# Optimization experiments

Measured on AMD Instinct MI355X. Metric: run time of the kernel, lower is better.

## Reference

```python
import jax, jax.numpy as jnp
import numpy as np

N_NODES = 50000
N_EDGES = 800000
IN_DIM = 128
HID = 128
N_GRAPHS = 256
N_CLASSES = 2
ALPHA = 0.2  # leaky relu slope
EPS_BN = 1e-5


def setup_inputs() -> dict:
    key = jax.random.key(0)
    ks = jax.random.split(key, 24)
    adjacency = jax.random.randint(ks[0], (2, N_EDGES), 0, N_NODES, dtype=jnp.int32)
    input_feature = jax.random.normal(ks[1], (N_NODES, IN_DIM), dtype=jnp.float32)
    graph_indicator = jnp.sort(jax.random.randint(ks[2], (N_NODES,), 0, N_GRAPHS, dtype=jnp.int32))
    labels = jax.random.randint(ks[3], (N_GRAPHS,), 0, N_CLASSES, dtype=jnp.int64)
    s = 0.05
    params = {
        'W1': jax.random.normal(ks[4], (IN_DIM, HID), jnp.float32) * s,
        'a1': jax.random.normal(ks[5], (2 * HID,), jnp.float32) * s,
        'bn2_g': jnp.ones((HID,), jnp.float32),
        'bn2_b': jnp.zeros((HID,), jnp.float32),
        'W2': jax.random.normal(ks[6], (HID, HID), jnp.float32) * s,
        'a2': jax.random.normal(ks[7], (2 * HID,), jnp.float32) * s,
        'bn3_g': jnp.ones((HID,), jnp.float32),
        'bn3_b': jnp.zeros((HID,), jnp.float32),
        'W3': jax.random.normal(ks[8], (HID, HID), jnp.float32) * s,
        'a3': jax.random.normal(ks[9], (2 * HID,), jnp.float32) * s,
        'fc1_w': jax.random.normal(ks[10], (HID, 2 * HID), jnp.float32) * s,
        'fc1_b': jnp.zeros((2 * HID,), jnp.float32),
        'fc2_w': jax.random.normal(ks[11], (2 * HID, HID), jnp.float32) * s,
        'fc2_b': jnp.zeros((HID,), jnp.float32),
        'fc3_w': jax.random.normal(ks[12], (HID, N_CLASSES), jnp.float32) * s,
        'fc3_b': jnp.zeros((N_CLASSES,), jnp.float32),
    }
    return dict(adjacency=adjacency, input_feature=input_feature,
                graph_indicator=graph_indicator, labels=labels, **params)


def _batchnorm(x, g, b):
    # training-mode BatchNorm1d over node dim (biased variance)
    mu = jnp.mean(x, axis=0)
    var = jnp.mean((x - mu) ** 2, axis=0)
    return (x - mu) * jax.lax.rsqrt(var + EPS_BN) * g + b


def _sp_gat(x, src, dst, W, a):
    # pyGAT SpGraphAttentionLayer (dropout disabled / eval mode)
    h = x @ W                                # [N, F]
    F = h.shape[1]
    e_src = h @ a[:F]                        # [N]
    e_dst = h @ a[F:]                        # [N]
    e = e_src[src] + e_dst[dst]              # [E]
    ee = jnp.exp(-jax.nn.leaky_relu(e, ALPHA))
    rowsum = jax.ops.segment_sum(ee, src, num_segments=N_NODES)          # [N]
    num = jax.ops.segment_sum(ee[:, None] * h[dst], src, num_segments=N_NODES)  # [N, F]
    h_prime = num / (rowsum[:, None] + 1e-16)
    return jax.nn.elu(h_prime)


def reference(adjacency, input_feature, graph_indicator, labels,
              W1, a1, bn2_g, bn2_b, W2, a2, bn3_g, bn3_b, W3, a3,
              fc1_w, fc1_b, fc2_w, fc2_b, fc3_w, fc3_b):
    src, dst = adjacency[0], adjacency[1]
    # bn1 output is discarded in the original forward
    x = _sp_gat(input_feature, src, dst, W1, a1)
    x = _batchnorm(x, bn2_g, bn2_b)
    x = _sp_gat(x, src, dst, W2, a2)
    x = _batchnorm(x, bn3_g, bn3_b)
    x = _sp_gat(x, src, dst, W3, a3)
    # pooling_sum_4tensor: per-graph sum pooling
    pooled = jax.ops.segment_sum(x, graph_indicator, num_segments=N_GRAPHS)  # [G, F]
    x = jax.nn.relu(pooled @ fc1_w + fc1_b)
    x = jax.nn.relu(x @ fc2_w + fc2_b)
    logits = x @ fc3_w + fc3_b
    return logits
```

## Files before the change

### kernel.cpp

```cpp
#include <hip/hip_runtime.h>
#include <hip/hip_bf16.h>

#define N_NODES 50000
#define N_EDGES 800000
#define FD 128
#define N_GRAPHS 256
#define NPART 6250

typedef unsigned short u16;
typedef short bf16x8 __attribute__((ext_vector_type(8)));
typedef float f32x4 __attribute__((ext_vector_type(4)));

__device__ __forceinline__ u16 f2bf(float v) {
    __hip_bfloat16 h = __float2bfloat16(v);
    union { __hip_bfloat16 hh; u16 u; } c; c.hh = h; return c.u;
}
__device__ __forceinline__ float bf2f(u16 r) {
    return __uint_as_float(((unsigned int)r) << 16);
}

__global__ __launch_bounds__(256) void count_deg_part_k(const int* __restrict__ src,
                                                        int* __restrict__ cnt, int E) {
    int part = blockIdx.x & 7;
    int lo = part * NPART, hi = lo + NPART;
    int stride = (gridDim.x >> 3) * 256;
    for (int e = (blockIdx.x >> 3) * 256 + threadIdx.x; e < E; e += stride) {
        int s = src[e];
        if (s >= lo && s < hi) atomicAdd(&cnt[s], 1);
    }
}

__global__ __launch_bounds__(256) void fill_csr_part_k(const int* __restrict__ src,
                                                       const int* __restrict__ dst,
                                                       int* __restrict__ cur,
                                                       int* __restrict__ edst, int E) {
    int part = blockIdx.x & 7;
    int lo = part * NPART, hi = lo + NPART;
    int stride = (gridDim.x >> 3) * 256;
    for (int e = (blockIdx.x >> 3) * 256 + threadIdx.x; e < E; e += stride) {
        int s = src[e];
        if (s >= lo && s < hi) {
            int p = atomicAdd(&cur[s], 1);
            edst[p] = dst[e];
        }
    }
}

__global__ __launch_bounds__(256) void scan1_k(const int* __restrict__ cnt,
                                               int* __restrict__ bsum, int M,
                                               float* __restrict__ bnbuf,
                                               float* __restrict__ pooled) {
    int i = blockIdx.x * 256 + threadIdx.x;
    int v = (i < M) ? cnt[i] : 0;
    __shared__ int l[256];
    l[threadIdx.x] = v;
    __syncthreads();
    for (int s = 128; s > 0; s >>= 1) {
        if (threadIdx.x < s) l[threadIdx.x] += l[threadIdx.x + s];
        __syncthreads();
    }
    if (threadIdx.x == 0) bsum[blockIdx.x] = l[0];
    if (blockIdx.x == 0) {
        bnbuf[threadIdx.x] = 0.f; bnbuf[threadIdx.x + 256] = 0.f;
        for (int k = threadIdx.x; k < N_GRAPHS * FD; k += 256) pooled[k] = 0.f;
    }
}

__global__ __launch_bounds__(256) void scan3_k(const int* __restrict__ cnt,
                                               const int* __restrict__ bsum,
                                               int* __restrict__ offs,
                                               int* __restrict__ cur, int M, int NB) {
    int i = blockIdx.x * 256 + threadIdx.x;
    int tid = threadIdx.x;
    __shared__ int bs[256];
    bs[tid] = (tid < NB) ? bsum[tid] : 0;
    __syncthreads();
    for (int off = 1; off < 256; off <<= 1) {
        int t = (tid >= off) ? bs[tid - off] : 0;
        __syncthreads();
        bs[tid] += t;
        __syncthreads();
    }
    int base = (blockIdx.x == 0) ? 0 : bs[blockIdx.x - 1];
    int v = (i < M) ? cnt[i] : 0;
    __shared__ int l[256];
    l[tid] = v;
    __syncthreads();
    for (int off = 1; off < 256; off <<= 1) {
        int t = (tid >= off) ? l[tid - off] : 0;
        __syncthreads();
        l[tid] += t;
        __syncthreads();
    }
    int excl = l[tid] - v + base;
    if (i < M) { offs[i] = excl; cur[i] = excl; }
    if (i == M - 1) offs[M] = excl + v;
}

__global__ __launch_bounds__(128) void wprep1_k(const float* __restrict__ W,
                                                u16* __restrict__ Wt,
                                                float* __restrict__ cvec) {
    int n = blockIdx.x, k = threadIdx.x;
    Wt[(size_t)n * FD + k] = f2bf(W[(size_t)k * FD + n]);
    if (k == 0) cvec[n] = 0.f;
}

__global__ __launch_bounds__(128) void bnfw_k(const float* __restrict__ W,
                                              const float* __restrict__ sums,
                                              const float* __restrict__ sumsq,
                                              const float* __restrict__ g,
                                              const float* __restrict__ b,
                                              float invN,
                                              u16* __restrict__ Wt,
                                              float* __restrict__ cvec) {
    int n = blockIdx.x, k = threadIdx.x;
    __shared__ float scs[128], shs[128], l[128];
    float mu = sums[k] * invN;
    float var = sumsq[k] * invN - mu * mu;
    float sc = g[k] * rsqrtf(var + 1e-5f);
    scs[k] = sc;
    shs[k] = b[k] - mu * sc;
    __syncthreads();
    float w = W[(size_t)k * FD + n];
    Wt[(size_t)n * FD + k] = f2bf(scs[k] * w);
    l[k] = shs[k] * w;
    __syncthreads();
    for (int s = 64; s > 0; s >>= 1) {
        if (k < s) l[k] += l[k + s];
        __syncthreads();
    }
    if (k == 0) cvec[n] = l[0];
}

__global__ __launch_bounds__(256) void gemm_mfma_k(const float* __restrict__ Xf,
                                                   const u16* __restrict__ Xb,
                                                   int use_f32,
                                                   const u16* __restrict__ Wt,
                                                   const float* __restrict__ cvec,
                                                   const float* __restrict__ avec,
                                                   u16* __restrict__ Hb,
                                                   float* __restrict__ es,
                                                   float* __restrict__ ed, int M) {
    __shared__ u16 As[64][136];
    __shared__ u16 Bs[128][136];
    __shared__ float sa_s[128], sa_d[128], cv[128];
    int tid = threadIdx.x;
    if (tid < 128) { sa_s[tid] = avec[tid]; sa_d[tid] = avec[128 + tid]; cv[tid] = cvec[tid]; }
    int row0 = blockIdx.x * 64;
    {
        int n = tid >> 1, k0 = (tid & 1) * 64;
        const uint4* s = (const uint4*)(Wt + (size_t)n * FD + k0);
#pragma unroll
        for (int u = 0; u < 8; u++) *(uint4*)&Bs[n][k0 + u * 8] = s[u];
    }
    {
        int r = tid >> 2, k0 = (tid & 3) * 32;
        int grow = row0 + r;
        if (grow < M) {
            if (use_f32) {
                const float4* s = (const float4*)(Xf + (size_t)grow * FD + k0);
#pragma unroll
                for (int u = 0; u < 8; u++) {
                    float4 v = s[u];
                    ushort4 o;
                    o.x = f2bf(v.x); o.y = f2bf(v.y); o.z = f2bf(v.z); o.w = f2bf(v.w);
                    *(ushort4*)&As[r][k0 + u * 4] = o;
                }
            } else {
                const uint4* s = (const uint4*)(Xb + (size_t)grow * FD + k0);
#pragma unroll
                for (int u = 0; u < 4; u++) *(uint4*)&As[r][k0 + u * 8] = s[u];
            }
        } else {
            uint4 z = make_uint4(0, 0, 0, 0);
#pragma unroll
            for (int u = 0; u < 4; u++) *(uint4*)&As[r][k0 + u * 8] = z;
        }
    }
    __syncthreads();

    int wave = tid >> 6, lane = tid & 63;
    int quad = lane >> 4, n16 = lane & 15;
    int rbase = wave * 16;
    f32x4 acc[8];
    f32x4 zz = {0.f, 0.f, 0.f, 0.f};
#pragma unroll
    for (int t = 0; t < 8; t++) acc[t] = zz;

#pragma unroll
    for (int kk = 0; kk < 128; kk += 32) {
        bf16x8 a = *(const bf16x8*)&As[rbase + n16][kk + quad * 8];
#pragma unroll
        for (int t = 0; t < 8; t++) {
            bf16x8 b = *(const bf16x8*)&Bs[t * 16 + n16][kk + quad * 8];
            acc[t] = __builtin_amdgcn_mfma_f32_16x16x32_bf16(a, b, acc[t], 0, 0, 0);
        }
    }

#pragma unroll
    for (int reg = 0; reg < 4; reg++) {
        int grow = row0 + rbase + quad * 4 + reg;
        float vals[8];
        float ps = 0.f, pd = 0.f;
#pragma unroll
        for (int t = 0; t < 8; t++) {
            float v = acc[t][reg] + cv[t * 16 + n16];
            vals[t] = v;
            ps += v * sa_s[t * 16 + n16];
            pd += v * sa_d[t * 16 + n16];
        }
#pragma unroll
        for (int o = 8; o > 0; o >>= 1) { ps += __shfl_xor(ps, o); pd += __shfl_xor(pd, o); }
        if (grow < M) {
            if (n16 == 0) { es[grow] = ps; ed[grow] = pd; }
#pragma unroll
            for (int t = 0; t < 8; t++)
                Hb[(size_t)grow * FD + t * 16 + n16] = f2bf(vals[t]);
        }
    }
}

#define EW(dd) ({ float _ev = esv + ed_[dd]; float _lr = _ev > 0.f ? _ev : 0.2f * _ev; __expf(-_lr); })
#define GACC(rr, ww) do { \
    acc0 += (ww) * __uint_as_float((rr).x << 16); \
    acc1 += (ww) * __uint_as_float((rr).x & 0xffff0000u); \
    acc2 += (ww) * __uint_as_float((rr).y << 16); \
    acc3 += (ww) * __uint_as_float((rr).y & 0xffff0000u); \
    acc4 += (ww) * __uint_as_float((rr).z << 16); \
    acc5 += (ww) * __uint_as_float((rr).z & 0xffff0000u); \
    acc6 += (ww) * __uint_as_float((rr).w << 16); \
    acc7 += (ww) * __uint_as_float((rr).w & 0xffff0000u); } while (0)

__global__ __launch_bounds__(256) void agg_k(const u16* __restrict__ Hb,
                                             const float* __restrict__ es_,
                                             const float* __restrict__ ed_,
                                             const int* __restrict__ offs,
                                             const int* __restrict__ edst,
                                             u16* __restrict__ Out, int M) {
    int node = __builtin_amdgcn_readfirstlane((int)((blockIdx.x * blockDim.x + threadIdx.x) >> 6));
    int lane = threadIdx.x & 63;
    if (node >= M) return;
    int g = lane >> 4;
    int p = lane & 15;
    int s0 = offs[node], s1 = offs[node + 1];
    float esv = es_[node];
    const uint4* Hq = (const uint4*)Hb;
    float acc0 = 0.f, acc1 = 0.f, acc2 = 0.f, acc3 = 0.f;
    float acc4 = 0.f, acc5 = 0.f, acc6 = 0.f, acc7 = 0.f;
    float rs = 0.f;
    int e = s0;
    for (; e + 8 <= s1; e += 8) {
        int d0 = __builtin_amdgcn_readfirstlane(edst[e]);
        int d1 = __builtin_amdgcn_readfirstlane(edst[e + 1]);
        int d2 = __builtin_amdgcn_readfirstlane(edst[e + 2]);
        int d3 = __builtin_amdgcn_readfirstlane(edst[e + 3]);
        int d4 = __builtin_amdgcn_readfirstlane(edst[e + 4]);
        int d5 = __builtin_amdgcn_readfirstlane(edst[e + 5]);
        int d6 = __builtin_amdgcn_readfirstlane(edst[e + 6]);
        int d7 = __builtin_amdgcn_readfirstlane(edst[e + 7]);
        int dgA = g == 0 ? d0 : (g == 1 ? d1 : (g == 2 ? d2 : d3));
        int dgB = g == 0 ? d4 : (g == 1 ? d5 : (g == 2 ? d6 : d7));
        uint4 rA = Hq[(size_t)dgA * 16 + p];
        uint4 rB = Hq[(size_t)dgB * 16 + p];
        float w0 = EW(d0), w1 = EW(d1), w2 = EW(d2), w3 = EW(d3);
        float w4 = EW(d4), w5 = EW(d5), w6 = EW(d6), w7 = EW(d7);
        rs += w0 + w1 + w2 + w3 + w4 + w5 + w6 + w7;
        float wgA = g == 0 ? w0 : (g == 1 ? w1 : (g == 2 ? w2 : w3));
        float wgB = g == 0 ? w4 : (g == 1 ? w5 : (g == 2 ? w6 : w7));
        GACC(rA, wgA);
        GACC(rB, wgB);
    }
    while (e < s1) {
        int m = s1 - e;
        if (m > 4) m = 4;
        int d0 = __builtin_amdgcn_readfirstlane(edst[e]);
        int d1 = m > 1 ? __builtin_amdgcn_readfirstlane(edst[e + 1]) : d0;
        int d2 = m > 2 ? __builtin_amdgcn_readfirstlane(edst[e + 2]) : d0;
        int d3 = m > 3 ? __builtin_amdgcn_readfirstlane(edst[e + 3]) : d0;
        float w0 = EW(d0);
        float w1 = m > 1 ? EW(d1) : 0.f;
        float w2 = m > 2 ? EW(d2) : 0.f;
        float w3 = m > 3 ? EW(d3) : 0.f;
        rs += w0 + w1 + w2 + w3;
        int dgA = g == 0 ? d0 : (g == 1 ? d1 : (g == 2 ? d2 : d3));
        float wgA = g == 0 ? w0 : (g == 1 ? w1 : (g == 2 ? w2 : w3));
        uint4 rA = Hq[(size_t)dgA * 16 + p];
        GACC(rA, wgA);
        e += m;
    }
#pragma unroll
    for (int o = 16; o < 64; o <<= 1) {
        acc0 += __shfl_xor(acc0, o); acc1 += __shfl_xor(acc1, o);
        acc2 += __shfl_xor(acc2, o); acc3 += __shfl_xor(acc3, o);
        acc4 += __shfl_xor(acc4, o); acc5 += __shfl_xor(acc5, o);
        acc6 += __shfl_xor(acc6, o); acc7 += __shfl_xor(acc7, o);
    }
    if (g == 0) {
        float inv = 1.f / (rs + 1e-16f);
        float v0 = acc0 * inv, v1 = acc1 * inv, v2 = acc2 * inv, v3 = acc3 * inv;
        float v4 = acc4 * inv, v5 = acc5 * inv, v6 = acc6 * inv, v7 = acc7 * inv;
        v0 = v0 > 0.f ? v0 : (__expf(v0) - 1.f);
        v1 = v1 > 0.f ? v1 : (__expf(v1) - 1.f);
        v2 = v2 > 0.f ? v2 : (__expf(v2) - 1.f);
        v3 = v3 > 0.f ? v3 : (__expf(v3) - 1.f);
        v4 = v4 > 0.f ? v4 : (__expf(v4) - 1.f);
        v5 = v5 > 0.f ? v5 : (__expf(v5) - 1.f);
        v6 = v6 > 0.f ? v6 : (__expf(v6) - 1.f);
        v7 = v7 > 0.f ? v7 : (__expf(v7) - 1.f);
        uint4 o4;
        o4.x = ((unsigned int)f2bf(v1) << 16) | f2bf(v0);
        o4.y = ((unsigned int)f2bf(v3) << 16) | f2bf(v2);
        o4.z = ((unsigned int)f2bf(v5) << 16) | f2bf(v4);
        o4.w = ((unsigned int)f2bf(v7) << 16) | f2bf(v6);
        ((uint4*)Out)[(size_t)node * 16 + p] = o4;
    }
}

__global__ void bnstats_b_k(const u16* __restrict__ Xb, float* __restrict__ sums,
                            float* __restrict__ sumsq, int M) {
    int f = threadIdx.x & 127;
    int half = threadIdx.x >> 7;
    float s1 = 0.f, s2 = 0.f;
    for (int r = blockIdx.x * 2 + half; r < M; r += gridDim.x * 2) {
        float v = bf2f(Xb[(size_t)r * FD + f]);
        s1 += v; s2 += v * v;
    }
    __shared__ float l1[256], l2[256];
    l1[threadIdx.x] = s1; l2[threadIdx.x] = s2;
    __syncthreads();
    if (half == 0) {
        atomicAdd(&sums[f], l1[f] + l1[f + 128]);
        atomicAdd(&sumsq[f], l2[f] + l2[f + 128]);
    }
}

__global__ void pool_k(const u16* __restrict__ Xb, const int* __restrict__ gi,
                       float* __restrict__ pooled, int M) {
    int f = threadIdx.x & 127;
    int half = threadIdx.x >> 7;
    int r0 = blockIdx.x * 128 + half;
    int rend = min(blockIdx.x * 128 + 128, M);
    int curg = -1; float acc = 0.f;
    for (int r = r0; r < rend; r += 2) {
        int g = gi[r];
        if (g != curg) {
            if (curg >= 0) atomicAdd(&pooled[(size_t)curg * FD + f], acc);
            curg = g; acc = 0.f;
        }
        acc += bf2f(Xb[(size_t)r * FD + f]);
    }
    if (curg >= 0) atomicAdd(&pooled[(size_t)curg * FD + f], acc);
}

__global__ __launch_bounds__(256) void mlp_k(const float* __restrict__ pooled,
                                             const float* __restrict__ fc1w, const float* __restrict__ fc1b,
                                             const float* __restrict__ fc2w, const float* __restrict__ fc2b,
                                             const float* __restrict__ fc3w, const float* __restrict__ fc3b,
                                             float* __restrict__ out) {
    int g = blockIdx.x, j = threadIdx.x;
    __shared__ float x[128], t1[256], t2[128], p0[128], p1[128];
    if (j < 128) x[j] = pooled[(size_t)g * FD + j];
    __syncthreads();
    float s = fc1b[j];
    for (int k = 0; k < 128; k++) s += x[k] * fc1w[(size_t)k * 256 + j];
    t1[j] = fmaxf(s, 0.f);
    __syncthreads();
    if (j < 128) {
        float s2 = fc2b[j];
        for (int k = 0; k < 256; k++) s2 += t1[k] * fc2w[(size_t)k * 128 + j];
        t2[j] = fmaxf(s2, 0.f);
    }
    __syncthreads();
    if (j < 128) { p0[j] = t2[j] * fc3w[j * 2]; p1[j] = t2[j] * fc3w[j * 2 + 1]; }
    __syncthreads();
    for (int s3 = 64; s3 > 0; s3 >>= 1) {
        if (j < s3) { p0[j] += p0[j + s3]; p1[j] += p1[j + s3]; }
        __syncthreads();
    }
    if (j == 0) { out[g * 2] = p0[0] + fc3b[0]; out[g * 2 + 1] = p1[0] + fc3b[1]; }
}

extern "C" void kernel_launch(void* const* d_in, const int* in_sizes, int n_in,
                              void* d_out, int out_size, void* d_ws, size_t ws_size,
                              hipStream_t stream) {
    const int*   adj  = (const int*)d_in[0];
    const float* xin  = (const float*)d_in[1];
    const int*   gi   = (const int*)d_in[2];
    const float* W1   = (const float*)d_in[4];
    const float* a1   = (const float*)d_in[5];
    const float* bn2g = (const float*)d_in[6];
    const float* bn2b = (const float*)d_in[7];
    const float* W2   = (const float*)d_in[8];
    const float* a2   = (const float*)d_in[9];
    const float* bn3g = (const float*)d_in[10];
    const float* bn3b = (const float*)d_in[11];
    const float* W3   = (const float*)d_in[12];
    const float* a3   = (const float*)d_in[13];
    const float* fc1w = (const float*)d_in[14];
    const float* fc1b = (const float*)d_in[15];
    const float* fc2w = (const float*)d_in[16];
    const float* fc2b = (const float*)d_in[17];
    const float* fc3w = (const float*)d_in[18];
    const float* fc3b = (const float*)d_in[19];
    float* out = (float*)d_out;

    const int N = N_NODES, E = N_EDGES, G = N_GRAPHS;

    u16*   Xb     = (u16*)d_ws;
    u16*   Hb     = Xb + (size_t)N * FD;
    u16*   Wt     = Hb + (size_t)N * FD;
    float* es     = (float*)(Wt + FD * FD);
    float* ed     = es + N;
    float* bnbuf  = ed + N;
    float* sumsA  = bnbuf;
    float* sumsqA = bnbuf + 128;
    float* sumsB  = bnbuf + 256;
    float* sumsqB = bnbuf + 384;
    float* cvec   = bnbuf + 512;
    float* pooled = cvec + FD;
    int*   degcnt = (int*)(pooled + (size_t)G * FD);
    int*   offs   = degcnt + N;
    int*   cur    = offs + (N + 2);
    int*   bsum   = cur + N;
    int*   edst   = bsum + 256;

    const int* srcp = adj;
    const int* dstp = adj + E;

    const int NB = (N + 255) / 256;

    hipMemsetAsync(degcnt, 0, (size_t)N * sizeof(int), stream);
    count_deg_part_k<<<8 * 392, 256, 0, stream>>>(srcp, degcnt, E);
    scan1_k<<<NB, 256, 0, stream>>>(degcnt, bsum, N, bnbuf, pooled);
    scan3_k<<<NB, 256, 0, stream>>>(degcnt, bsum, offs, cur, N, NB);
    fill_csr_part_k<<<8 * 392, 256, 0, stream>>>(srcp, dstp, cur, edst, E);

    const int gemm_grid = (N + 63) / 64;
    const int wave_grid = (N + 3) / 4;
    const float invN = 1.0f / (float)N;

    wprep1_k<<<FD, 128, 0, stream>>>(W1, Wt, cvec);
    gemm_mfma_k<<<gemm_grid, 256, 0, stream>>>(xin, Xb, 1, Wt, cvec, a1, Hb, es, ed, N);
    agg_k<<<wave_grid, 256, 0, stream>>>(Hb, es, ed, offs, edst, Xb, N);
    bnstats_b_k<<<256, 256, 0, stream>>>(Xb, sumsA, sumsqA, N);

    bnfw_k<<<FD, 128, 0, stream>>>(W2, sumsA, sumsqA, bn2g, bn2b, invN, Wt, cvec);
    gemm_mfma_k<<<gemm_grid, 256, 0, stream>>>(nullptr, Xb, 0, Wt, cvec, a2, Hb, es, ed, N);
    agg_k<<<wave_grid, 256, 0, stream>>>(Hb, es, ed, offs, edst, Xb, N);
    bnstats_b_k<<<256, 256, 0, stream>>>(Xb, sumsB, sumsqB, N);

    bnfw_k<<<FD, 128, 0, stream>>>(W3, sumsB, sumsqB, bn3g, bn3b, invN, Wt, cvec);
    gemm_mfma_k<<<gemm_grid, 256, 0, stream>>>(nullptr, Xb, 0, Wt, cvec, a3, Hb, es, ed, N);
    agg_k<<<wave_grid, 256, 0, stream>>>(Hb, es, ed, offs, edst, Xb, N);

    pool_k<<<(N + 127) / 128, 256, 0, stream>>>(Xb, gi, pooled, N);
    mlp_k<<<G, 256, 0, stream>>>(pooled, fc1w, fc1b, fc2w, fc2b, fc3w, fc3b, out);
}
```

Measured before the change: 433.0 us.

## Split H into feature quarter-planes and precompute edge weights in separate pass

Result: slower. 569.6 us (+31.6%).

```diff
diff --git a/kernel.cpp b/kernel.cpp
--- a/kernel.cpp
+++ b/kernel.cpp
@@ -138,7 +138,7 @@
                                                    const u16* __restrict__ Wt,
                                                    const float* __restrict__ cvec,
                                                    const float* __restrict__ avec,
-                                                   u16* __restrict__ Hb,
+                                                   u16* __restrict__ Hq,
                                                    float* __restrict__ es,
                                                    float* __restrict__ ed, int M) {
     __shared__ u16 As[64][136];
@@ -215,39 +215,63 @@
             if (n16 == 0) { es[grow] = ps; ed[grow] = pd; }
 #pragma unroll
             for (int t = 0; t < 8; t++)
-                Hb[(size_t)grow * FD + t * 16 + n16] = f2bf(vals[t]);
-        }
-    }
-}
-
-#define EW(dd) ({ float _ev = esv + ed_[dd]; float _lr = _ev > 0.f ? _ev : 0.2f * _ev; __expf(-_lr); })
-#define GACC(rr, ww) do { \
-    acc0 += (ww) * __uint_as_float((rr).x << 16); \
-    acc1 += (ww) * __uint_as_float((rr).x & 0xffff0000u); \
-    acc2 += (ww) * __uint_as_float((rr).y << 16); \
-    acc3 += (ww) * __uint_as_float((rr).y & 0xffff0000u); \
-    acc4 += (ww) * __uint_as_float((rr).z << 16); \
-    acc5 += (ww) * __uint_as_float((rr).z & 0xffff0000u); \
-    acc6 += (ww) * __uint_as_float((rr).w << 16); \
-    acc7 += (ww) * __uint_as_float((rr).w & 0xffff0000u); } while (0)
-
-__global__ __launch_bounds__(256) void agg_k(const u16* __restrict__ Hb,
-                                             const float* __restrict__ es_,
-                                             const float* __restrict__ ed_,
-                                             const int* __restrict__ offs,
-                                             const int* __restrict__ edst,
-                                             u16* __restrict__ Out, int M) {
-    int node = __builtin_amdgcn_readfirstlane((int)((blockIdx.x * blockDim.x + threadIdx.x) >> 6));
+                Hq[(size_t)(t >> 1) * M * 32 + (size_t)grow * 32 + (t & 1) * 16 + n16] = f2bf(vals[t]);
+        }
+    }
+}
+
+__global__ __launch_bounds__(256) void ee_k(const float* __restrict__ es_,
+                                            const float* __restrict__ ed_,
+                                            const int* __restrict__ offs,
+                                            const int* __restrict__ edst,
+                                            float* __restrict__ wbuf,
+                                            float* __restrict__ rowsum, int M) {
+    int wave = (blockIdx.x * blockDim.x + threadIdx.x) >> 6;
     int lane = threadIdx.x & 63;
+    if (wave >= M) return;
+    int s0 = offs[wave], s1 = offs[wave + 1];
+    float esv = es_[wave];
+    float rs = 0.f;
+    for (int base = s0; base < s1; base += 64) {
+        int m = s1 - base; if (m > 64) m = 64;
+        if (lane < m) {
+            int d = edst[base + lane];
+            float ev = esv + ed_[d];
+            float lr = ev > 0.f ? ev : 0.2f * ev;
+            float w = __expf(-lr);
+            wbuf[base + lane] = w;
+            rs += w;
+        }
+    }
+#pragma unroll
+    for (int o = 32; o > 0; o >>= 1) rs += __shfl_xor(rs, o);
+    if (lane == 0) rowsum[wave] = rs;
+}
+
+#define QACC(rr, ww) do { \
+    acc0 += (ww) * __uint_as_float((rr) << 16); \
+    acc1 += (ww) * __uint_as_float((rr) & 0xffff0000u); } while (0)
+
+__global__ __launch_bounds__(256) void agg_q_k(const u16* __restrict__ Hq,
+                                               const float* __restrict__ wbuf,
+                                               const float* __restrict__ rowsum,
+                                               const int* __restrict__ offs,
+                                               const int* __restrict__ edst,
+                                               u16* __restrict__ Out, int M) {
+    int b = blockIdx.x;
+    int q = b & 3;
+    int r = (b >> 2) & 1;
+    int v = b >> 3;
+    int wavein = threadIdx.x >> 6;
+    int node = __builtin_amdgcn_readfirstlane((v * 2 + r) * 4 + wavein);
     if (node >= M) return;
+    int lane = threadIdx.x & 63;
     int g = lane >> 4;
     int p = lane & 15;
     int s0 = offs[node], s1 = offs[node + 1];
-    float esv = es_[node];
-    const uint4* Hq = (const uint4*)Hb;
-    float acc0 = 0.f, acc1 = 0.f, acc2 = 0.f, acc3 = 0.f;
-    float acc4 = 0.f, acc5 = 0.f, acc6 = 0.f, acc7 = 0.f;
-    float rs = 0.f;
+    const unsigned int* plane = (const unsigned int*)(Hq + (size_t)q * M * 32);
+    const int* wbi = (const int*)wbuf;
+    float acc0 = 0.f, acc1 = 0.f;
     int e = s0;
     for (; e + 8 <= s1; e += 8) {
         int d0 = __builtin_amdgcn_readfirstlane(edst[e]);
@@ -258,61 +282,51 @@
         int d5 = __builtin_amdgcn_readfirstlane(edst[e + 5]);
         int d6 = __builtin_amdgcn_readfirstlane(edst[e + 6]);
         int d7 = __builtin_amdgcn_readfirstlane(edst[e + 7]);
+        float w0 = __int_as_float(__builtin_amdgcn_readfirstlane(wbi[e]));
+        float w1 = __int_as_float(__builtin_amdgcn_readfirstlane(wbi[e + 1]));
+        float w2 = __int_as_float(__builtin_amdgcn_readfirstlane(wbi[e + 2]));
+        float w3 = __int_as_float(__builtin_amdgcn_readfirstlane(wbi[e + 3]));
+        float w4 = __int_as_float(__builtin_amdgcn_readfirstlane(wbi[e + 4]));
+        float w5 = __int_as_float(__builtin_amdgcn_readfirstlane(wbi[e + 5]));
+        float w6 = __int_as_float(__builtin_amdgcn_readfirstlane(wbi[e + 6]));
+        float w7 = __int_as_float(__builtin_amdgcn_readfirstlane(wbi[e + 7]));
         int dgA = g == 0 ? d0 : (g == 1 ? d1 : (g == 2 ? d2 : d3));
         int dgB = g == 0 ? d4 : (g == 1 ? d5 : (g == 2 ? d6 : d7));
-        uint4 rA = Hq[(size_t)dgA * 16 + p];
-        uint4 rB = Hq[(size_t)dgB * 16 + p];
-        float w0 = EW(d0), w1 = EW(d1), w2 = EW(d2), w3 = EW(d3);
-        float w4 = EW(d4), w5 = EW(d5), w6 = EW(d6), w7 = EW(d7);
-        rs += w0 + w1 + w2 + w3 + w4 + w5 + w6 + w7;
         float wgA = g == 0 ? w0 : (g == 1 ? w1 : (g == 2 ? w2 : w3));
         float wgB = g == 0 ? w4 : (g == 1 ? w5 : (g == 2 ? w6 : w7));
-        GACC(rA, wgA);
-        GACC(rB, wgB);
+        unsigned int rA = plane[(size_t)dgA * 16 + p];
+        unsigned int rB = plane[(size_t)dgB * 16 + p];
+        QACC(rA, wgA);
+        QACC(rB, wgB);
     }
     while (e < s1) {
-        int m = s1 - e;
-        if (m > 4) m = 4;
+        int m = s1 - e; if (m > 4) m = 4;
         int d0 = __builtin_amdgcn_readfirstlane(edst[e]);
         int d1 = m > 1 ? __builtin_amdgcn_readfirstlane(edst[e + 1]) : d0;
         int d2 = m > 2 ? __builtin_amdgcn_readfirstlane(edst[e + 2]) : d0;
         int d3 = m > 3 ? __builtin_amdgcn_readfirstlane(edst[e + 3]) : d0;
-        float w0 = EW(d0);
-        float w1 = m > 1 ? EW(d1) : 0.f;
-        float w2 = m > 2 ? EW(d2) : 0.f;
-        float w3 = m > 3 ? EW(d3) : 0.f;
-        rs += w0 + w1 + w2 + w3;
+        float w0 = __int_as_float(__builtin_amdgcn_readfirstlane(wbi[e]));
+        float w1 = m > 1 ? __int_as_float(__builtin_amdgcn_readfirstlane(wbi[e + 1])) : 0.f;
+        float w2 = m > 2 ? __int_as_float(__builtin_amdgcn_readfirstlane(wbi[e + 2])) : 0.f;
+        float w3 = m > 3 ? __int_as_float(__builtin_amdgcn_readfirstlane(wbi[e + 3])) : 0.f;
         int dgA = g == 0 ? d0 : (g == 1 ? d1 : (g == 2 ? d2 : d3));
         float wgA = g == 0 ? w0 : (g == 1 ? w1 : (g == 2 ? w2 : w3));
-        uint4 rA = Hq[(size_t)dgA * 16 + p];
-        GACC(rA, wgA);
+        unsigned int rA = plane[(size_t)dgA * 16 + p];
+        QACC(rA, wgA);
         e += m;
     }
 #pragma unroll
     for (int o = 16; o < 64; o <<= 1) {
-        acc0 += __shfl_xor(acc0, o); acc1 += __shfl_xor(acc1, o);
-        acc2 += __shfl_xor(acc2, o); acc3 += __shfl_xor(acc3, o);
-        acc4 += __shfl_xor(acc4, o); acc5 += __shfl_xor(acc5, o);
-        acc6 += __shfl_xor(acc6, o); acc7 += __shfl_xor(acc7, o);
+        acc0 += __shfl_xor(acc0, o);
+        acc1 += __shfl_xor(acc1, o);
     }
     if (g == 0) {
-        float inv = 1.f / (rs + 1e-16f);
-        float v0 = acc0 * inv, v1 = acc1 * inv, v2 = acc2 * inv, v3 = acc3 * inv;
-        float v4 = acc4 * inv, v5 = acc5 * inv, v6 = acc6 * inv, v7 = acc7 * inv;
+        float inv = 1.f / (rowsum[node] + 1e-16f);
+        float v0 = acc0 * inv, v1 = acc1 * inv;
         v0 = v0 > 0.f ? v0 : (__expf(v0) - 1.f);
         v1 = v1 > 0.f ? v1 : (__expf(v1) - 1.f);
-        v2 = v2 > 0.f ? v2 : (__expf(v2) - 1.f);
-        v3 = v3 > 0.f ? v3 : (__expf(v3) - 1.f);
-        v4 = v4 > 0.f ? v4 : (__expf(v4) - 1.f);
-        v5 = v5 > 0.f ? v5 : (__expf(v5) - 1.f);
-        v6 = v6 > 0.f ? v6 : (__expf(v6) - 1.f);
-        v7 = v7 > 0.f ? v7 : (__expf(v7) - 1.f);
-        uint4 o4;
-        o4.x = ((unsigned int)f2bf(v1) << 16) | f2bf(v0);
-        o4.y = ((unsigned int)f2bf(v3) << 16) | f2bf(v2);
-        o4.z = ((unsigned int)f2bf(v5) << 16) | f2bf(v4);
-        o4.w = ((unsigned int)f2bf(v7) << 16) | f2bf(v6);
-        ((uint4*)Out)[(size_t)node * 16 + p] = o4;
+        ((unsigned int*)Out)[(size_t)node * 64 + q * 16 + p] =
+            ((unsigned int)f2bf(v1) << 16) | f2bf(v0);
     }
 }
 
@@ -407,11 +421,13 @@
     const int N = N_NODES, E = N_EDGES, G = N_GRAPHS;
 
     u16*   Xb     = (u16*)d_ws;
-    u16*   Hb     = Xb + (size_t)N * FD;
-    u16*   Wt     = Hb + (size_t)N * FD;
+    u16*   Hq     = Xb + (size_t)N * FD;
+    u16*   Wt     = Hq + (size_t)N * FD;
     float* es     = (float*)(Wt + FD * FD);
     float* ed     = es + N;
-    float* bnbuf  = ed + N;
+    float* rowsum = ed + N;
+    float* wbuf   = rowsum + N;
+    float* bnbuf  = wbuf + E;
     float* sumsA  = bnbuf;
     float* sumsqA = bnbuf + 128;
     float* sumsB  = bnbuf + 256;
@@ -437,21 +453,25 @@
 
     const int gemm_grid = (N + 63) / 64;
     const int wave_grid = (N + 3) / 4;
+    const int aggq_grid = (((N + 3) / 4 + 1) / 2) * 8;
     const float invN = 1.0f / (float)N;
 
     wprep1_k<<<FD, 128, 0, stream>>>(W1, Wt, cvec);
-    gemm_mfma_k<<<gemm_grid, 256, 0, stream>>>(xin, Xb, 1, Wt, cvec, a1, Hb, es, ed, N);
-    agg_k<<<wave_grid, 256, 0, stream>>>(Hb, es, ed, offs, edst, Xb, N);
+    gemm_mfma_k<<<gemm_grid, 256, 0, stream>>>(xin, Xb, 1, Wt, cvec, a1, Hq, es, ed, N);
+    ee_k<<<wave_grid, 256, 0, stream>>>(es, ed, offs, edst, wbuf, rowsum, N);
+    agg_q_k<<<aggq_grid, 256, 0, stream>>>(Hq, wbuf, rowsum, offs, edst, Xb, N);
     bnstats_b_k<<<256, 256, 0, stream>>>(Xb, sumsA, sumsqA, N);
 
     bnfw_k<<<FD, 128, 0, stream>>>(W2, sumsA, sumsqA, bn2g, bn2b, invN, Wt, cvec);
-    gemm_mfma_k<<<gemm_grid, 256, 0, stream>>>(nullptr, Xb, 0, Wt, cvec, a2, Hb, es, ed, N);
-    agg_k<<<wave_grid, 256, 0, stream>>>(Hb, es, ed, offs, edst, Xb, N);
+    gemm_mfma_k<<<gemm_grid, 256, 0, stream>>>(nullptr, Xb, 0, Wt, cvec, a2, Hq, es, ed, N);
+    ee_k<<<wave_grid, 256, 0, stream>>>(es, ed, offs, edst, wbuf, rowsum, N);
+    agg_q_k<<<aggq_grid, 256, 0, stream>>>(Hq, wbuf, rowsum, offs, edst, Xb, N);
     bnstats_b_k<<<256, 256, 0, stream>>>(Xb, sumsB, sumsqB, N);
 
     bnfw_k<<<FD, 128, 0, stream>>>(W3, sumsB, sumsqB, bn3g, bn3b, invN, Wt, cvec);
-    gemm_mfma_k<<<gemm_grid, 256, 0, stream>>>(nullptr, Xb, 0, Wt, cvec, a3, Hb, es, ed, N);
-    agg_k<<<wave_grid, 256, 0, stream>>>(Hb, es, ed, offs, edst, Xb, N);
+    gemm_mfma_k<<<gemm_grid, 256, 0, stream>>>(nullptr, Xb, 0, Wt, cvec, a3, Hq, es, ed, N);
+    ee_k<<<wave_grid, 256, 0, stream>>>(es, ed, offs, edst, wbuf, rowsum, N);
+    agg_q_k<<<aggq_grid, 256, 0, stream>>>(Hq, wbuf, rowsum, offs, edst, Xb, N);
 
     pool_k<<<(N + 127) / 128, 256, 0, stream>>>(Xb, gi, pooled, N);
     mlp_k<<<G, 256, 0, stream>>>(pooled, fc1w, fc1b, fc2w, fc2b, fc3w, fc3b, out);
```
